# Optimization experiments

Measured on AMD Instinct MI355X. Metric: run time of the kernel, lower is better.

The kernel has to match this reference:

```python
import jax, jax.numpy as jnp
import numpy as np
import math

HEAD = 4
HEAD_DIM = 16
K_ATT = 7
PAD_ATT = 3  # (dilation*(kernel_att-1)+1)//2 with dilation=1, kernel_att=7
K_CONV = 3


def closest_factor_to_sqrt(n):
    if n <= 1:
        return n
    sqrt_n = int(math.sqrt(n))
    if sqrt_n * sqrt_n == n:
        return sqrt_n
    best, best_diff = 1, float('inf')
    for i in range(sqrt_n, 0, -1):
        if n % i == 0:
            diff = abs(i - n // i)
            if diff < best_diff:
                best_diff, best = diff, i
    return best


def setup_inputs() -> dict:
    key = jax.random.key(0)
    ks = jax.random.split(key, 10)
    Cin, Cout = 64, 64
    x = jax.random.normal(ks[0], (2, Cin, 8, 32, 32), dtype=jnp.float32)
    w1 = jax.random.normal(ks[1], (Cout, Cin), dtype=jnp.float32) * 0.05
    b1 = jax.random.normal(ks[2], (Cout,), dtype=jnp.float32) * 0.01
    w2 = jax.random.normal(ks[3], (Cout, Cin), dtype=jnp.float32) * 0.05
    b2 = jax.random.normal(ks[4], (Cout,), dtype=jnp.float32) * 0.01
    w3 = jax.random.normal(ks[5], (Cout, Cin), dtype=jnp.float32) * 0.05
    b3 = jax.random.normal(ks[6], (Cout,), dtype=jnp.float32) * 0.01
    wp = jax.random.normal(ks[7], (HEAD_DIM, 3), dtype=jnp.float32) * 0.05
    bp = jnp.zeros((HEAD_DIM,), dtype=jnp.float32)
    wfc = jax.random.normal(ks[8], (K_CONV * K_CONV, 3 * HEAD), dtype=jnp.float32) * 0.05
    # dep_conv init per reset_parameters(): identity shift kernels, zero bias
    ident = jnp.eye(K_CONV * K_CONV, dtype=jnp.float32).reshape(K_CONV * K_CONV, K_CONV, K_CONV)
    wdep = jnp.tile(ident[None], (Cout, 1, 1, 1))  # (Cout, 9, 3, 3), groups=head_dim
    bdep = jnp.zeros((Cout,), dtype=jnp.float32)
    rate1 = jnp.array(0.5, dtype=jnp.float32)
    rate2 = jnp.array(0.5, dtype=jnp.float32)
    return {'x': x, 'w1': w1, 'b1': b1, 'w2': w2, 'b2': b2, 'w3': w3, 'b3': b3,
            'wp': wp, 'bp': bp, 'wfc': wfc, 'wdep': wdep, 'bdep': bdep,
            'rate1': rate1, 'rate2': rate2}


def _forward(x, w1, b1, w2, b2, w3, b3, wp, bp, wfc, wdep, bdep, rate1, rate2):
    conv1x1 = lambda t, wm, bias: jnp.einsum('oc,bcdwh->bodwh', wm, t) + bias[None, :, None, None, None]
    q = conv1x1(x, w1, b1)
    k = conv1x1(x, w2, b2)
    v = conv1x1(x, w3, b3)
    b, C, d, w, h = q.shape
    scaling = HEAD_DIM ** -0.5
    fh = closest_factor_to_sqrt(d)
    fw = d // fh
    H2, W2 = fh * h, fw * w  # flat reshape of (d, w, h) -> (H2, W2)

    # position encoding, torch position(d, h, w) -> (1, 3, d, w, h)
    loc_d = jnp.broadcast_to(jnp.linspace(-1.0, 1.0, d)[:, None, None], (d, w, h))
    loc_w = jnp.broadcast_to(jnp.linspace(-1.0, 1.0, w)[None, :, None], (d, w, h))
    loc_h = jnp.broadcast_to(jnp.linspace(-1.0, 1.0, h)[None, None, :], (d, w, h))
    loc = jnp.stack([loc_d, loc_w, loc_h], 0)[None].astype(x.dtype)
    pe = (jnp.einsum('oc,bcdwh->bodwh', wp, loc) + bp[None, :, None, None, None])
    pe = pe.reshape(1, HEAD_DIM, H2, W2)

    q_att = (q * scaling).reshape(b * HEAD, HEAD_DIM, H2, W2)
    k_att = k.reshape(b * HEAD, HEAD_DIM, H2, W2)
    v_att = v.reshape(b * HEAD, HEAD_DIM, H2, W2)

    def unfold(t):
        # nn.Unfold(kernel=7, stride=1) after ReflectionPad2d(3): (N, C, 49, H2, W2)
        p = jnp.pad(t, ((0, 0), (0, 0), (PAD_ATT, PAD_ATT), (PAD_ATT, PAD_ATT)), mode='reflect')
        return jnp.stack([p[:, :, i:i + H2, j:j + W2]
                          for i in range(K_ATT) for j in range(K_ATT)], axis=2)

    unfold_k = unfold(k_att)            # (b*head, hd, 49, H2, W2)
    unfold_rpe = unfold(pe)             # (1, hd, 49, H2, W2)
    scores = unfold_k + pe[:, :, None] - unfold_rpe
    att = jnp.einsum('nchw,nckhw->nkhw', q_att, scores)  # sum over head_dim
    att = jax.nn.softmax(att, axis=1)   # softmax over 49 window positions
    out_att = jnp.einsum('nkhw,nckhw->nchw', att, unfold(v_att))
    out_att = out_att.reshape(b, C, d, w, h)

    # conv-mixing branch
    L = d * w * h
    qkv = jnp.concatenate([q.reshape(b, HEAD, HEAD_DIM, L),
                           k.reshape(b, HEAD, HEAD_DIM, L),
                           v.reshape(b, HEAD, HEAD_DIM, L)], axis=1)  # (b, 3*head, hd, L)
    # fc: 1x1x1 conv over the 3*head channel axis (torch applies it unbatched after permute)
    f_all = jnp.einsum('oc,bcml->boml', wfc, qkv)         # (b, 9, hd, L)
    f_conv = f_all.reshape(b, K_CONV * K_CONV * HEAD_DIM, d, h * w)
    out_conv = jax.lax.conv_general_dilated(
        f_conv, wdep, window_strides=(1, 1), padding=[(1, 1), (1, 1)],
        dimension_numbers=('NCHW', 'OIHW', 'NCHW'), feature_group_count=HEAD_DIM)
    out_conv = out_conv + bdep[None, :, None, None]
    out_conv = out_conv.reshape(b, C, d, w, h)

    return rate1 * out_att + rate2 * out_conv


def reference(x, w1, b1, w2, b2, w3, b3, wp, bp, wfc, wdep, bdep, rate1, rate2):
    return _forward(x, w1, b1, w2, b2, w3, b3, wp, bp, wfc, wdep, bdep, rate1, rate2)
```

## Files before the change

### kernel.cpp

```cpp
#include <hip/hip_runtime.h>


__global__ __launch_bounds__(512) void qkvf_kernel(
    const float* __restrict__ x,
    const float* __restrict__ w1, const float* __restrict__ b1,
    const float* __restrict__ w2, const float* __restrict__ b2,
    const float* __restrict__ w3, const float* __restrict__ b3,
    const float* __restrict__ wfc,
    float* __restrict__ q, float* __restrict__ k, float* __restrict__ v,
    float* __restrict__ f)
{
    __shared__ float xs[64][128];
    __shared__ float wlds[3][32][64];

    int bx    = blockIdx.x;
    int ltile = bx & 63;
    int half  = (bx >> 6) & 1;
    int b     = bx >> 7;
    int l0    = ltile * 128;
    int hdb   = half * 8;

    for (int t = threadIdx.x; t < 1536; t += 512) {
        int mat = t >> 9;
        int r   = t & 511;
        int cl  = r >> 4;
        int col = r & 15;
        int hh = cl >> 3, hdl = cl & 7;
        int c  = hh * 16 + hdb + hdl;
        const float* src = (mat == 0) ? w1 : (mat == 1) ? w2 : w3;
        ((float4*)wlds)[t] = ((const float4*)src)[c * 16 + col];
    }
    const float4* xg = (const float4*)(x + (size_t)b * 64 * 8192);
    for (int t = threadIdx.x; t < 2048; t += 512) {
        int ci = t >> 5, col = t & 31;
        ((float4*)xs)[t] = xg[ci * 2048 + (l0 >> 2) + col];
    }
    __syncthreads();

    int lane = threadIdx.x & 63;
    int wv   = __builtin_amdgcn_readfirstlane(threadIdx.x >> 6);
    int hd   = hdb + wv;
    int ll   = 2 * lane;

    float qa[4][2], ka[4][2], va[4][2];
#pragma unroll
    for (int hh = 0; hh < 4; ++hh) {
        int c = hh * 16 + hd;
        qa[hh][0] = qa[hh][1] = b1[c];
        ka[hh][0] = ka[hh][1] = b2[c];
        va[hh][0] = va[hh][1] = b3[c];
    }

#pragma unroll 4
    for (int c4 = 0; c4 < 16; ++c4) {
        float2 xv[4];
#pragma unroll
        for (int u = 0; u < 4; ++u)
            xv[u] = *(const float2*)&xs[c4 * 4 + u][ll];
#pragma unroll
        for (int hh = 0; hh < 4; ++hh) {
            int cl = hh * 8 + wv;
            float4 wq = *(const float4*)&wlds[0][cl][c4 * 4];
            float4 wk = *(const float4*)&wlds[1][cl][c4 * 4];
            float4 wx = *(const float4*)&wlds[2][cl][c4 * 4];
            qa[hh][0] = fmaf(wq.x, xv[0].x, qa[hh][0]);
            qa[hh][1] = fmaf(wq.x, xv[0].y, qa[hh][1]);
            qa[hh][0] = fmaf(wq.y, xv[1].x, qa[hh][0]);
            qa[hh][1] = fmaf(wq.y, xv[1].y, qa[hh][1]);
            qa[hh][0] = fmaf(wq.z, xv[2].x, qa[hh][0]);
            qa[hh][1] = fmaf(wq.z, xv[2].y, qa[hh][1]);
            qa[hh][0] = fmaf(wq.w, xv[3].x, qa[hh][0]);
            qa[hh][1] = fmaf(wq.w, xv[3].y, qa[hh][1]);

            ka[hh][0] = fmaf(wk.x, xv[0].x, ka[hh][0]);
            ka[hh][1] = fmaf(wk.x, xv[0].y, ka[hh][1]);
            ka[hh][0] = fmaf(wk.y, xv[1].x, ka[hh][0]);
            ka[hh][1] = fmaf(wk.y, xv[1].y, ka[hh][1]);
            ka[hh][0] = fmaf(wk.z, xv[2].x, ka[hh][0]);
            ka[hh][1] = fmaf(wk.z, xv[2].y, ka[hh][1]);
            ka[hh][0] = fmaf(wk.w, xv[3].x, ka[hh][0]);
            ka[hh][1] = fmaf(wk.w, xv[3].y, ka[hh][1]);

            va[hh][0] = fmaf(wx.x, xv[0].x, va[hh][0]);
            va[hh][1] = fmaf(wx.x, xv[0].y, va[hh][1]);
            va[hh][0] = fmaf(wx.y, xv[1].x, va[hh][0]);
            va[hh][1] = fmaf(wx.y, xv[1].y, va[hh][1]);
            va[hh][0] = fmaf(wx.z, xv[2].x, va[hh][0]);
            va[hh][1] = fmaf(wx.z, xv[2].y, va[hh][1]);
            va[hh][0] = fmaf(wx.w, xv[3].x, va[hh][0]);
            va[hh][1] = fmaf(wx.w, xv[3].y, va[hh][1]);
        }
    }

#pragma unroll
    for (int hh = 0; hh < 4; ++hh) {
        int c = hh * 16 + hd;
        size_t o = (size_t)(b * 64 + c) * 8192 + l0 + ll;
        *(float2*)&q[o] = make_float2(qa[hh][0] * 0.25f, qa[hh][1] * 0.25f);
        *(float2*)&k[o] = make_float2(ka[hh][0], ka[hh][1]);
        *(float2*)&v[o] = make_float2(va[hh][0], va[hh][1]);
    }

#pragma unroll
    for (int m = 0; m < 9; ++m) {
        float a0 = 0.f, a1 = 0.f;
#pragma unroll
        for (int hh = 0; hh < 4; ++hh) {
            a0 = fmaf(wfc[m * 12 + 0 + hh], qa[hh][0], a0);
            a1 = fmaf(wfc[m * 12 + 0 + hh], qa[hh][1], a1);
            a0 = fmaf(wfc[m * 12 + 4 + hh], ka[hh][0], a0);
            a1 = fmaf(wfc[m * 12 + 4 + hh], ka[hh][1], a1);
            a0 = fmaf(wfc[m * 12 + 8 + hh], va[hh][0], a0);
            a1 = fmaf(wfc[m * 12 + 8 + hh], va[hh][1], a1);
        }
        size_t o = ((size_t)(b * 9 + m) * 16 + hd) * 8192 + l0 + ll;
        *(float2*)&f[o] = make_float2(a0, a1);
    }
}

__global__ __launch_bounds__(512, 4) void att_kernel(
    const float* __restrict__ q, const float* __restrict__ k,
    const float* __restrict__ v,
    const float* __restrict__ wp, const float* __restrict__ bp,
    const float* __restrict__ rate1p, float* __restrict__ out)
{
    __shared__ float kp[22 * 22 * 20];
    __shared__ float vt[22 * 22 * 20];

    int bx = blockIdx.x;
    int xt = bx & 7;
    int yt = (bx >> 3) & 3;
    int n  = bx >> 5;
    int head = n & 3;
    int b    = n >> 2;
    int y0 = yt * 16, x0 = xt * 16;

    const int NELEM = 16 * 22 * 22;
    for (int e = threadIdx.x; e < NELEM; e += 512) {
        int tx  = e % 22;
        int rem = e / 22;
        int ty  = rem % 22;
        int c   = rem / 22;
        int sy = y0 + ty - 3; if (sy < 0) sy = -sy; else if (sy >= 64)  sy = 126 - sy;
        int sx = x0 + tx - 3; if (sx < 0) sx = -sx; else if (sx >= 128) sx = 254 - sx;
        int l = sy * 128 + sx;
        size_t o = (size_t)(b * 64 + head * 16 + c) * 8192 + l;
        int dd = l >> 10, r2 = l & 1023, ww = r2 >> 5, hh = r2 & 31;
        float ld = dd * (2.0f / 7.0f)  - 1.0f;
        float lw = ww * (2.0f / 31.0f) - 1.0f;
        float lh = hh * (2.0f / 31.0f) - 1.0f;
        float pe = bp[c];
        pe = fmaf(wp[c * 3 + 0], ld, pe);
        pe = fmaf(wp[c * 3 + 1], lw, pe);
        pe = fmaf(wp[c * 3 + 2], lh, pe);
        int li = (ty * 22 + tx) * 20 + c;
        kp[li] = k[o] - pe;
        vt[li] = v[o];
    }
    __syncthreads();

    int pix  = threadIdx.x >> 1;
    int part = threadIdx.x & 1;
    int tx = pix & 15, ty = pix >> 4;
    int l = (y0 + ty) * 128 + (x0 + tx);
    int cb = part * 8;

    float qc[8];
#pragma unroll
    for (int c = 0; c < 8; ++c)
        qc[c] = q[(size_t)(b * 64 + head * 16 + cb + c) * 8192 + l];

    float lg[49];
#pragma unroll
    for (int i = 0; i < 7; ++i)
#pragma unroll
        for (int j = 0; j < 7; ++j) {
            const float4* p =
                (const float4*)&kp[((ty + i) * 22 + tx + j) * 20 + cb];
            float4 a = p[0], b4 = p[1];
            float acc =      qc[0] * a.x;
            acc = fmaf(qc[1], a.y,  acc); acc = fmaf(qc[2], a.z,  acc);
            acc = fmaf(qc[3], a.w,  acc); acc = fmaf(qc[4], b4.x, acc);
            acc = fmaf(qc[5], b4.y, acc); acc = fmaf(qc[6], b4.z, acc);
            acc = fmaf(qc[7], b4.w, acc);
            lg[i * 7 + j] = acc;
        }
#pragma unroll
    for (int kk = 0; kk < 49; ++kk)
        lg[kk] += __shfl_xor(lg[kk], 1, 64);

    float mx = lg[0];
#pragma unroll
    for (int kk = 1; kk < 49; ++kk) mx = fmaxf(mx, lg[kk]);
    float se = 0.f;
#pragma unroll
    for (int kk = 0; kk < 49; ++kk) { lg[kk] = __expf(lg[kk] - mx); se += lg[kk]; }
    float scale = rate1p[0] / se;

    float oc[8];
#pragma unroll
    for (int c = 0; c < 8; ++c) oc[c] = 0.f;
#pragma unroll
    for (int i = 0; i < 7; ++i)
#pragma unroll
        for (int j = 0; j < 7; ++j) {
            float wgt = lg[i * 7 + j];
            const float4* p =
                (const float4*)&vt[((ty + i) * 22 + tx + j) * 20 + cb];
            float4 a = p[0], b4 = p[1];
            oc[0] = fmaf(wgt, a.x,  oc[0]); oc[1] = fmaf(wgt, a.y,  oc[1]);
            oc[2] = fmaf(wgt, a.z,  oc[2]); oc[3] = fmaf(wgt, a.w,  oc[3]);
            oc[4] = fmaf(wgt, b4.x, oc[4]); oc[5] = fmaf(wgt, b4.y, oc[5]);
            oc[6] = fmaf(wgt, b4.z, oc[6]); oc[7] = fmaf(wgt, b4.w, oc[7]);
        }

#pragma unroll
    for (int c = 0; c < 8; ++c)
        out[(size_t)(b * 64 + head * 16 + cb + c) * 8192 + l] = oc[c] * scale;
}

__global__ __launch_bounds__(256) void conv_kernel(
    const float* __restrict__ f,
    const float* __restrict__ wdep, const float* __restrict__ bdep,
    const float* __restrict__ rate2p, float* __restrict__ out)
{
    __shared__ float ft[9][8][66];

    int bx = blockIdx.x;
    int xt = bx & 15;
    int g  = (bx >> 4) & 15;
    int b  = bx >> 8;
    int x0 = xt * 64;

    const int NE = 9 * 8 * 66;
    for (int e = threadIdx.x; e < NE; e += 256) {
        int xx  = e % 66;
        int rem = e / 66;
        int y = rem % 8, i = rem / 8;
        int gx = x0 + xx - 1;
        float val = 0.f;
        if (gx >= 0 && gx < 1024) {
            int c144 = g * 9 + i;
            val = f[((size_t)(b * 144 + c144)) * 8192 + y * 1024 + gx];
        }
        ft[i][y][xx] = val;
    }
    __syncthreads();

    int xl = threadIdx.x & 63;
    int op = __builtin_amdgcn_readfirstlane(threadIdx.x >> 6);
    int o  = g * 4 + op;
    float rate2 = rate2p[0];

    float acc[8];
#pragma unroll
    for (int y = 0; y < 8; ++y) acc[y] = 0.f;

    for (int i = 0; i < 9; ++i) {
        float fr[10][3];
#pragma unroll
        for (int dx = 0; dx < 3; ++dx) { fr[0][dx] = 0.f; fr[9][dx] = 0.f; }
#pragma unroll
        for (int y = 0; y < 8; ++y)
#pragma unroll
            for (int dx = 0; dx < 3; ++dx)
                fr[y + 1][dx] = ft[i][y][xl + dx];
#pragma unroll
        for (int ky = 0; ky < 3; ++ky)
#pragma unroll
            for (int kx = 0; kx < 3; ++kx) {
                float wvv = wdep[((o * 9 + i) * 3 + ky) * 3 + kx];
#pragma unroll
                for (int y = 0; y < 8; ++y)
                    acc[y] = fmaf(wvv, fr[y + ky][kx], acc[y]);
            }
    }

    float bd = bdep[o];
#pragma unroll
    for (int y = 0; y < 8; ++y) {
        size_t idx = (size_t)(b * 64 + o) * 8192 + y * 1024 + x0 + xl;
        out[idx] = out[idx] + rate2 * (acc[y] + bd);
    }
}

extern "C" void kernel_launch(void* const* d_in, const int* in_sizes, int n_in,
                              void* d_out, int out_size, void* d_ws, size_t ws_size,
                              hipStream_t stream)
{
    (void)in_sizes; (void)n_in; (void)out_size; (void)ws_size;
    const float* x     = (const float*)d_in[0];
    const float* w1    = (const float*)d_in[1];
    const float* b1    = (const float*)d_in[2];
    const float* w2    = (const float*)d_in[3];
    const float* b2    = (const float*)d_in[4];
    const float* w3    = (const float*)d_in[5];
    const float* b3    = (const float*)d_in[6];
    const float* wp    = (const float*)d_in[7];
    const float* bp    = (const float*)d_in[8];
    const float* wfc   = (const float*)d_in[9];
    const float* wdep  = (const float*)d_in[10];
    const float* bdep  = (const float*)d_in[11];
    const float* rate1 = (const float*)d_in[12];
    const float* rate2 = (const float*)d_in[13];
    float* out = (float*)d_out;

    float* wsf = (float*)d_ws;
    float* q = wsf;
    float* k = wsf + 1048576;
    float* v = wsf + 2097152;
    float* f = wsf + 3145728;

    qkvf_kernel<<<256, 512, 0, stream>>>(x, w1, b1, w2, b2, w3, b3, wfc,
                                         q, k, v, f);
    att_kernel <<<256, 512, 0, stream>>>(q, k, v, wp, bp, rate1, out);
    conv_kernel<<<512, 256, 0, stream>>>(f, wdep, bdep, rate2, out);
}
```

Before: 120.2 us.

## Fuse attention and depthwise conv kernels into one tile-based kernel

Merges the attention kernel and the depthwise conv kernel into a single kernel. The attention result is held in shared memory and the conv input tile is loaded into reused shared memory, so each output is written once. This removes one launch and the read-modify-write pass over the output. In exchange it uses more shared memory per block (about 99KB), drops the occupancy hint, and uses a remapped conv tiling whose halo loads are less coalesced.

```diff
diff --git a/kernel.cpp b/kernel.cpp
--- a/kernel.cpp
+++ b/kernel.cpp
@@ -118,14 +118,18 @@
     }
 }
 
-__global__ __launch_bounds__(512, 4) void att_kernel(
+__global__ __launch_bounds__(512) void attconv_kernel(
     const float* __restrict__ q, const float* __restrict__ k,
-    const float* __restrict__ v,
+    const float* __restrict__ v, const float* __restrict__ f,
     const float* __restrict__ wp, const float* __restrict__ bp,
-    const float* __restrict__ rate1p, float* __restrict__ out)
+    const float* __restrict__ wdep, const float* __restrict__ bdep,
+    const float* __restrict__ rate1p, const float* __restrict__ rate2p,
+    float* __restrict__ out)
 {
-    __shared__ float kp[22 * 22 * 20];
-    __shared__ float vt[22 * 22 * 20];
+    __shared__ float smem[20772];
+    __shared__ float att_buf[4096];
+    float* kp = smem;
+    float* vt = smem + 9680;
 
     int bx = blockIdx.x;
     int xt = bx & 7;
@@ -159,129 +163,148 @@
     }
     __syncthreads();
 
-    int pix  = threadIdx.x >> 1;
-    int part = threadIdx.x & 1;
-    int tx = pix & 15, ty = pix >> 4;
-    int l = (y0 + ty) * 128 + (x0 + tx);
-    int cb = part * 8;
-
-    float qc[8];
-#pragma unroll
-    for (int c = 0; c < 8; ++c)
-        qc[c] = q[(size_t)(b * 64 + head * 16 + cb + c) * 8192 + l];
-
-    float lg[49];
-#pragma unroll
-    for (int i = 0; i < 7; ++i)
-#pragma unroll
-        for (int j = 0; j < 7; ++j) {
-            const float4* p =
-                (const float4*)&kp[((ty + i) * 22 + tx + j) * 20 + cb];
-            float4 a = p[0], b4 = p[1];
-            float acc =      qc[0] * a.x;
-            acc = fmaf(qc[1], a.y,  acc); acc = fmaf(qc[2], a.z,  acc);
-            acc = fmaf(qc[3], a.w,  acc); acc = fmaf(qc[4], b4.x, acc);
-            acc = fmaf(qc[5], b4.y, acc); acc = fmaf(qc[6], b4.z, acc);
-            acc = fmaf(qc[7], b4.w, acc);
-            lg[i * 7 + j] = acc;
-        }
-#pragma unroll
-    for (int kk = 0; kk < 49; ++kk)
-        lg[kk] += __shfl_xor(lg[kk], 1, 64);
-
-    float mx = lg[0];
-#pragma unroll
-    for (int kk = 1; kk < 49; ++kk) mx = fmaxf(mx, lg[kk]);
-    float se = 0.f;
-#pragma unroll
-    for (int kk = 0; kk < 49; ++kk) { lg[kk] = __expf(lg[kk] - mx); se += lg[kk]; }
-    float scale = rate1p[0] / se;
-
-    float oc[8];
-#pragma unroll
-    for (int c = 0; c < 8; ++c) oc[c] = 0.f;
-#pragma unroll
-    for (int i = 0; i < 7; ++i)
-#pragma unroll
-        for (int j = 0; j < 7; ++j) {
-            float wgt = lg[i * 7 + j];
-            const float4* p =
-                (const float4*)&vt[((ty + i) * 22 + tx + j) * 20 + cb];
-            float4 a = p[0], b4 = p[1];
-            oc[0] = fmaf(wgt, a.x,  oc[0]); oc[1] = fmaf(wgt, a.y,  oc[1]);
-            oc[2] = fmaf(wgt, a.z,  oc[2]); oc[3] = fmaf(wgt, a.w,  oc[3]);
-            oc[4] = fmaf(wgt, b4.x, oc[4]); oc[5] = fmaf(wgt, b4.y, oc[5]);
-            oc[6] = fmaf(wgt, b4.z, oc[6]); oc[7] = fmaf(wgt, b4.w, oc[7]);
-        }
-
-#pragma unroll
-    for (int c = 0; c < 8; ++c)
-        out[(size_t)(b * 64 + head * 16 + cb + c) * 8192 + l] = oc[c] * scale;
-}
-
-__global__ __launch_bounds__(256) void conv_kernel(
-    const float* __restrict__ f,
-    const float* __restrict__ wdep, const float* __restrict__ bdep,
-    const float* __restrict__ rate2p, float* __restrict__ out)
-{
-    __shared__ float ft[9][8][66];
-
-    int bx = blockIdx.x;
-    int xt = bx & 15;
-    int g  = (bx >> 4) & 15;
-    int b  = bx >> 8;
-    int x0 = xt * 64;
-
-    const int NE = 9 * 8 * 66;
-    for (int e = threadIdx.x; e < NE; e += 256) {
-        int xx  = e % 66;
-        int rem = e / 66;
-        int y = rem % 8, i = rem / 8;
-        int gx = x0 + xx - 1;
+    {
+        int pix  = threadIdx.x >> 1;
+        int part = threadIdx.x & 1;
+        int tx = pix & 15, ty = pix >> 4;
+        int l = (y0 + ty) * 128 + (x0 + tx);
+        int cb = part * 8;
+
+        float qc[8];
+#pragma unroll
+        for (int c = 0; c < 8; ++c)
+            qc[c] = q[(size_t)(b * 64 + head * 16 + cb + c) * 8192 + l];
+
+        float lg[49];
+#pragma unroll
+        for (int i = 0; i < 7; ++i)
+#pragma unroll
+            for (int j = 0; j < 7; ++j) {
+                const float4* p =
+                    (const float4*)&kp[((ty + i) * 22 + tx + j) * 20 + cb];
+                float4 a = p[0], b4 = p[1];
+                float acc =      qc[0] * a.x;
+                acc = fmaf(qc[1], a.y,  acc); acc = fmaf(qc[2], a.z,  acc);
+                acc = fmaf(qc[3], a.w,  acc); acc = fmaf(qc[4], b4.x, acc);
+                acc = fmaf(qc[5], b4.y, acc); acc = fmaf(qc[6], b4.z, acc);
+                acc = fmaf(qc[7], b4.w, acc);
+                lg[i * 7 + j] = acc;
+            }
+#pragma unroll
+        for (int kk = 0; kk < 49; ++kk)
+            lg[kk] += __shfl_xor(lg[kk], 1, 64);
+
+        float mx = lg[0];
+#pragma unroll
+        for (int kk = 1; kk < 49; ++kk) mx = fmaxf(mx, lg[kk]);
+        float se = 0.f;
+#pragma unroll
+        for (int kk = 0; kk < 49; ++kk) { lg[kk] = __expf(lg[kk] - mx); se += lg[kk]; }
+        float scale = rate1p[0] / se;
+
+        float oc[8];
+#pragma unroll
+        for (int c = 0; c < 8; ++c) oc[c] = 0.f;
+#pragma unroll
+        for (int i = 0; i < 7; ++i)
+#pragma unroll
+            for (int j = 0; j < 7; ++j) {
+                float wgt = lg[i * 7 + j];
+                const float4* p =
+                    (const float4*)&vt[((ty + i) * 22 + tx + j) * 20 + cb];
+                float4 a = p[0], b4 = p[1];
+                oc[0] = fmaf(wgt, a.x,  oc[0]); oc[1] = fmaf(wgt, a.y,  oc[1]);
+                oc[2] = fmaf(wgt, a.z,  oc[2]); oc[3] = fmaf(wgt, a.w,  oc[3]);
+                oc[4] = fmaf(wgt, b4.x, oc[4]); oc[5] = fmaf(wgt, b4.y, oc[5]);
+                oc[6] = fmaf(wgt, b4.z, oc[6]); oc[7] = fmaf(wgt, b4.w, oc[7]);
+            }
+
+#pragma unroll
+        for (int c = 0; c < 8; ++c)
+            att_buf[(cb + c) * 256 + pix] = oc[c] * scale;
+    }
+    __syncthreads();
+
+    float* fs = smem;
+    const float* fb = f + (size_t)(b * 144 + 36 * head) * 8192;
+    int y2base = (y0 >> 3) - 1;
+    for (int e = threadIdx.x; e < 20736; e += 512) {
+        int c36 = e / 576;
+        int rem = e % 576;
+        int xo  = rem % 18;
+        int r   = rem / 18;
+        int s   = r & 7;
+        int y2r = r >> 3;
+        int y2  = y2base + y2r;
+        int x2  = s * 128 + x0 - 1 + xo;
         float val = 0.f;
-        if (gx >= 0 && gx < 1024) {
-            int c144 = g * 9 + i;
-            val = f[((size_t)(b * 144 + c144)) * 8192 + y * 1024 + gx];
-        }
-        ft[i][y][xx] = val;
+        if (y2 >= 0 && y2 < 8 && x2 >= 0 && x2 < 1024)
+            val = fb[(size_t)c36 * 8192 + y2 * 1024 + x2];
+        fs[c36 * 577 + rem] = val;
     }
     __syncthreads();
 
-    int xl = threadIdx.x & 63;
-    int op = __builtin_amdgcn_readfirstlane(threadIdx.x >> 6);
-    int o  = g * 4 + op;
+    int wv   = __builtin_amdgcn_readfirstlane(threadIdx.x >> 6);
+    int g    = wv >> 1;
+    int ch0  = 2 * wv;
+    int lane = threadIdx.x & 63;
+    int txc  = lane & 15;
+    int qq   = lane >> 4;
+
+    float cacc[2][2][2];
+#pragma unroll
+    for (int a0 = 0; a0 < 2; ++a0)
+#pragma unroll
+        for (int a1 = 0; a1 < 2; ++a1)
+#pragma unroll
+            for (int a2 = 0; a2 < 2; ++a2) cacc[a0][a1][a2] = 0.f;
+
+    for (int i = 0; i < 9; ++i) {
+        const float* fsl = &fs[(g * 9 + i) * 577];
+        float w0[9], w1[9];
+#pragma unroll
+        for (int t = 0; t < 9; ++t) {
+            w0[t] = wdep[((head * 16 + ch0)     * 9 + i) * 9 + t];
+            w1[t] = wdep[((head * 16 + ch0 + 1) * 9 + i) * 9 + t];
+        }
+#pragma unroll
+        for (int ss = 0; ss < 2; ++ss) {
+            int sl = qq + 4 * ss;
+            float fr[4][3];
+#pragma unroll
+            for (int r = 0; r < 4; ++r)
+#pragma unroll
+                for (int kx = 0; kx < 3; ++kx)
+                    fr[r][kx] = fsl[(r * 8 + sl) * 18 + txc + kx];
+#pragma unroll
+            for (int yl2 = 0; yl2 < 2; ++yl2)
+#pragma unroll
+                for (int ky = 0; ky < 3; ++ky)
+#pragma unroll
+                    for (int kx = 0; kx < 3; ++kx) {
+                        float fv = fr[yl2 + ky][kx];
+                        cacc[ss][yl2][0] = fmaf(w0[ky * 3 + kx], fv, cacc[ss][yl2][0]);
+                        cacc[ss][yl2][1] = fmaf(w1[ky * 3 + kx], fv, cacc[ss][yl2][1]);
+                    }
+        }
+    }
+
     float rate2 = rate2p[0];
-
-    float acc[8];
-#pragma unroll
-    for (int y = 0; y < 8; ++y) acc[y] = 0.f;
-
-    for (int i = 0; i < 9; ++i) {
-        float fr[10][3];
-#pragma unroll
-        for (int dx = 0; dx < 3; ++dx) { fr[0][dx] = 0.f; fr[9][dx] = 0.f; }
-#pragma unroll
-        for (int y = 0; y < 8; ++y)
-#pragma unroll
-            for (int dx = 0; dx < 3; ++dx)
-                fr[y + 1][dx] = ft[i][y][xl + dx];
-#pragma unroll
-        for (int ky = 0; ky < 3; ++ky)
-#pragma unroll
-            for (int kx = 0; kx < 3; ++kx) {
-                float wvv = wdep[((o * 9 + i) * 3 + ky) * 3 + kx];
-#pragma unroll
-                for (int y = 0; y < 8; ++y)
-                    acc[y] = fmaf(wvv, fr[y + ky][kx], acc[y]);
-            }
-    }
-
-    float bd = bdep[o];
-#pragma unroll
-    for (int y = 0; y < 8; ++y) {
-        size_t idx = (size_t)(b * 64 + o) * 8192 + y * 1024 + x0 + xl;
-        out[idx] = out[idx] + rate2 * (acc[y] + bd);
-    }
+    float bd0 = bdep[head * 16 + ch0];
+    float bd1 = bdep[head * 16 + ch0 + 1];
+#pragma unroll
+    for (int ss = 0; ss < 2; ++ss)
+#pragma unroll
+        for (int yl2 = 0; yl2 < 2; ++yl2) {
+            int ty = yl2 * 8 + qq + 4 * ss;
+            int p  = ty * 16 + txc;
+            size_t base = (size_t)(b * 64 + head * 16 + ch0) * 8192
+                          + (y0 + ty) * 128 + x0 + txc;
+            out[base] = att_buf[ch0 * 256 + p]
+                        + rate2 * (cacc[ss][yl2][0] + bd0);
+            out[base + 8192] = att_buf[(ch0 + 1) * 256 + p]
+                               + rate2 * (cacc[ss][yl2][1] + bd1);
+        }
 }
 
 extern "C" void kernel_launch(void* const* d_in, const int* in_sizes, int n_in,
@@ -311,8 +334,8 @@
     float* v = wsf + 2097152;
     float* f = wsf + 3145728;
 
-    qkvf_kernel<<<256, 512, 0, stream>>>(x, w1, b1, w2, b2, w3, b3, wfc,
-                                         q, k, v, f);
-    att_kernel <<<256, 512, 0, stream>>>(q, k, v, wp, bp, rate1, out);
-    conv_kernel<<<512, 256, 0, stream>>>(f, wdep, bdep, rate2, out);
+    qkvf_kernel  <<<256, 512, 0, stream>>>(x, w1, b1, w2, b2, w3, b3, wfc,
+                                           q, k, v, f);
+    attconv_kernel<<<256, 512, 0, stream>>>(q, k, v, f, wp, bp, wdep, bdep,
+                                            rate1, rate2, out);
 }
```

New measurement: 127.1 us. 5.8% more time.
